# Optimization experiments

Hardware: AMD Instinct MI355X
Metric: run time of the kernel (lower is better)

## Reference

```python
import jax, jax.numpy as jnp
import numpy as np

DIM = 128
HEADS = 4
DIM_HEAD = 32
N_EMBD = HEADS * DIM_HEAD  # 128
SCALE = DIM_HEAD ** -0.5


def conv2d(x, w, b):
    # NCHW conv, 3x3, stride 1, SAME padding (= padding=1 in torch)
    out = jax.lax.conv_general_dilated(
        x, w, window_strides=(1, 1), padding='SAME',
        dimension_numbers=('NCHW', 'OIHW', 'NCHW'))
    return out + b[None, :, None, None]


def conv_block(x, w1, b1, w2, b2):
    # Conv -> ReLU -> Conv (the to_q/to_k/to_v pattern)
    return conv2d(jax.nn.relu(conv2d(x, w1, b1)), w2, b2)


def setup_inputs() -> dict:
    key = jax.random.key(0)
    ks = jax.random.split(key, 20)
    B, C, S = 4, DIM, 32
    H, W = 128, 512
    wscale = 0.05

    def cw(k, cout, cin):
        return jax.random.normal(k, (cout, cin, 3, 3), jnp.float32) * wscale

    inp = {
        'x': jax.random.normal(ks[0], (B, C, S, S), jnp.float32),
        'y': jax.random.normal(ks[1], (B, C, H, W), jnp.float32),
        'u': jax.random.randint(ks[2], (B, S, S), 0, W),
        'q_w1': cw(ks[3], N_EMBD, DIM), 'q_b1': jnp.zeros((N_EMBD,), jnp.float32),
        'q_w2': cw(ks[4], N_EMBD, N_EMBD), 'q_b2': jnp.zeros((N_EMBD,), jnp.float32),
        'k_w1': cw(ks[5], N_EMBD, DIM), 'k_b1': jnp.zeros((N_EMBD,), jnp.float32),
        'k_w2': cw(ks[6], N_EMBD, N_EMBD), 'k_b2': jnp.zeros((N_EMBD,), jnp.float32),
        'v_w1': cw(ks[7], N_EMBD, DIM), 'v_b1': jnp.zeros((N_EMBD,), jnp.float32),
        'v_w2': cw(ks[8], N_EMBD, N_EMBD), 'v_b2': jnp.zeros((N_EMBD,), jnp.float32),
        'proj_w': cw(ks[9], DIM, N_EMBD), 'proj_b': jnp.zeros((DIM,), jnp.float32),
    }
    return inp


def reference(x, y, u, q_w1, q_b1, q_w2, q_b2, k_w1, k_b1, k_w2, k_b2,
              v_w1, v_b1, v_w2, v_b2, proj_w, proj_b):
    B, C, S, _ = x.shape
    _, _, H, W = y.shape
    SS = S * S

    # Q from the (B,C,S,S) query grid -> (B, S^2, n_embd)
    q = conv_block(x, q_w1, q_b1, q_w2, q_b2).reshape(B, N_EMBD, SS).transpose(0, 2, 1)

    # K, V from the (B,C,H,W) map
    k = conv_block(y, k_w1, k_b1, k_w2, k_b2)  # (B, E, H, W)
    v = conv_block(y, v_w1, v_b1, v_w2, v_b2)

    # Gather columns of K/V along W per query index u (clamped)
    uc = jnp.clip(u, 0, W - 1).astype(jnp.int32).reshape(B, 1, 1, SS)
    ks = jnp.take_along_axis(k, uc, axis=3).transpose(0, 3, 2, 1)  # (B, SS, H, E)
    vs = jnp.take_along_axis(v, uc, axis=3).transpose(0, 3, 2, 1)  # (B, SS, H, E)

    # Per-query attention over the H axis
    dot = SCALE * jnp.einsum('bqe,bqhe->bqh', q, ks)  # (B, SS, H)
    attn = jax.nn.softmax(dot, axis=-1)
    a = jnp.einsum('bqh,bqhe->bqe', attn, vs)  # (B, SS, E)

    a = a.transpose(0, 2, 1).reshape(B, N_EMBD, S, S)
    z = jax.nn.relu(conv2d(a, proj_w, proj_b))  # (B, DIM, S, S)
    return z
```

## Files before the change

kernel.cpp:

```cpp
#include <hip/hip_runtime.h>
#include <stdint.h>

typedef __attribute__((ext_vector_type(16))) float f32x16;
typedef __attribute__((ext_vector_type(8))) short s16x8;

__device__ inline short bf16b(float f) {
  uint32_t x = __float_as_uint(f);
  return (short)((x + 0x7fffu + ((x >> 16) & 1u)) >> 16);
}
__device__ inline float bfu(uint16_t u) { return __uint_as_float(((uint32_t)u) << 16); }

__device__ inline void gll16(const void* g, void* l) {
  __builtin_amdgcn_global_load_lds((const __attribute__((address_space(1))) void*)g,
                                   (__attribute__((address_space(3))) void*)l, 16, 0, 0);
}

__global__ __launch_bounds__(256) void packw_k(
    const float* w0, const float* w1, const float* w2, const float* w3,
    const float* w4, const float* w5, const float* w6, s16x8* dst) {
  const float* srcs[7] = {w0, w1, w2, w3, w4, w5, w6};
  const int widx = blockIdx.y;
  const float* src = srcs[widx];
  const int gid = blockIdx.x * 256 + threadIdx.x;
  const int lane = gid & 63, frag = gid >> 6;
  const int nblk = frag & 3, ks = (frag >> 2) & 1, chunk = (frag >> 3) & 3, tap = frag >> 5;
  const int co = nblk * 32 + (lane & 31);
  const int cib = chunk * 32 + ks * 16 + (lane >> 5) * 8;
  s16x8 v;
#pragma unroll
  for (int j = 0; j < 8; ++j)
    v[j] = bf16b(src[((size_t)co * 128 + cib + j) * 9 + tap]);
  dst[(size_t)widx * 18432 + (size_t)frag * 64 + lane] = v;
}

template <int TW>
__global__ __launch_bounds__(256) void nchw2nhwc_k(
    const float* __restrict__ in, uint16_t* __restrict__ out, int H, int W) {
  __shared__ float tile[128][TW + 1];
  const int b = blockIdx.z, h = blockIdx.y, w0 = blockIdx.x * TW;
  for (int idx = threadIdx.x; idx < 128 * TW; idx += 256) {
    int c = idx / TW, w = idx - c * TW;
    tile[c][w] = in[(((size_t)b * 128 + c) * H + h) * W + w0 + w];
  }
  __syncthreads();
  for (int idx = threadIdx.x; idx < TW * 16; idx += 256) {
    int w = idx >> 4, cg = idx & 15;
    s16x8 v;
#pragma unroll
    for (int j = 0; j < 8; ++j) v[j] = bf16b(tile[cg * 8 + j][w]);
    *reinterpret_cast<s16x8*>(out + ((((size_t)b * H + h) * W + w0 + w) << 7) + cg * 8) = v;
  }
}

template <int OMODE, bool RELU, typename Tout>
__global__ __launch_bounds__(256, 2) void convmf2_k(
    const uint16_t* __restrict__ in, const s16x8* __restrict__ wpk,
    const float* __restrict__ bias, Tout* __restrict__ out,
    const uint16_t* __restrict__ zp, int H, int W) {
  constexpr int CP = 34, RPCP = 10 * 34;
  constexpr int SLOTS = 4 * RPCP;
  constexpr int SPT = 6;
  __shared__ s16x8 lds[2][SPT * 256];
  const int b = blockIdx.z, r0 = blockIdx.y * 8, c0 = blockIdx.x * 32;
  const int tid = threadIdx.x, lane = tid & 63;
  const int wv = tid >> 6, wm = wv >> 1, wn = wv & 1;
  const int wbase = tid & 192;

  const uint16_t* gsrc[SPT];
#pragma unroll
  for (int i = 0; i < SPT; ++i) {
    const int s = tid + i * 256;
    const int kq = s / RPCP;
    const int rem = s - kq * RPCP;
    const int r = rem / CP, c = rem - r * CP;
    const int gr = r0 + r - 1, gc = c0 + c - 1;
    const bool ok = (s < SLOTS) && gr >= 0 && gr < H && gc >= 0 && gc < W;
    gsrc[i] = ok ? (in + (((size_t)b * H + gr) * W + gc) * 128 + kq * 8) : zp;
  }

#pragma unroll
  for (int i = 0; i < SPT; ++i) gll16(gsrc[i], &lds[0][wbase + i * 256]);

  f32x16 acc[4][2];
#pragma unroll
  for (int i = 0; i < 4; ++i)
#pragma unroll
    for (int j = 0; j < 2; ++j)
#pragma unroll
      for (int r = 0; r < 16; ++r) acc[i][j][r] = 0.f;

  const int rowb = wm * 4 * CP + (lane >> 5) * RPCP + (lane & 31);
  __syncthreads();

#pragma unroll 1
  for (int chunk = 0; chunk < 4; ++chunk) {
    const int cb = chunk & 1;
    if (chunk < 3) {
#pragma unroll
      for (int i = 0; i < SPT; ++i)
        gll16(gsrc[i] + (chunk + 1) * 32, &lds[cb ^ 1][wbase + i * 256]);
    }
    const s16x8* __restrict__ Lb = &lds[cb][rowb];
    const s16x8* __restrict__ wpc = wpk + ((size_t)chunk * 8 + wn * 2) * 64 + lane;
    s16x8 bwA[2], bwB[2];
    bwA[0] = wpc[0]; bwA[1] = wpc[64];
#pragma unroll
    for (int t9 = 0; t9 < 18; ++t9) {
      const int tap = t9 >> 1, ks = t9 & 1;
      const int ky = tap / 3, kx = tap - ky * 3;
      if (t9 < 17) {
        const int tn = t9 + 1, tapn = tn >> 1, ksn = tn & 1;
        s16x8* nx = (t9 & 1) ? bwA : bwB;
        nx[0] = wpc[tapn * 2048 + ksn * 256];
        nx[1] = wpc[tapn * 2048 + ksn * 256 + 64];
      }
      const s16x8* cw = (t9 & 1) ? bwB : bwA;
#pragma unroll
      for (int mf = 0; mf < 4; ++mf) {
        const s16x8 av = Lb[ks * (2 * RPCP) + (mf + ky) * CP + kx];
        acc[mf][0] = __builtin_amdgcn_mfma_f32_32x32x16_bf16(av, cw[0], acc[mf][0], 0, 0, 0);
        acc[mf][1] = __builtin_amdgcn_mfma_f32_32x32x16_bf16(av, cw[1], acc[mf][1], 0, 0, 0);
      }
    }
    if (chunk < 3) __syncthreads();
  }

#pragma unroll
  for (int nf = 0; nf < 2; ++nf) {
    const int co = wn * 64 + nf * 32 + (lane & 31);
    const float bv = bias[co];
#pragma unroll
    for (int mf = 0; mf < 4; ++mf) {
      const int gr = r0 + wm * 4 + mf;
#pragma unroll
      for (int reg = 0; reg < 16; ++reg) {
        const int gc = c0 + (reg & 3) + 8 * (reg >> 2) + 4 * (lane >> 5);
        float v = acc[mf][nf][reg] + bv;
        if (RELU) v = fmaxf(v, 0.f);
        size_t idx;
        if (OMODE == 0)      idx = (((size_t)b * H + gr) * W + gc) * 128 + co;
        else if (OMODE == 1) idx = (((size_t)b * W + gc) * H + gr) * 128 + co;
        else                 idx = (((size_t)b * 128 + co) * H + gr) * W + gc;
        if constexpr (sizeof(Tout) == 2) ((uint16_t*)out)[idx] = (uint16_t)bf16b(v);
        else out[idx] = v;
      }
    }
  }
}

__global__ __launch_bounds__(128) void attn_dot_k(
    const float* __restrict__ qg, const uint16_t* __restrict__ Kg,
    const int* __restrict__ u, float* __restrict__ pout) {
  const int bs = blockIdx.x;
  const int b = bs >> 10;
  const int tid = threadIdx.x;
  __shared__ float sq[128], sd[128];
  sq[tid] = qg[(size_t)bs * 128 + tid];
  int w = u[bs]; w = w < 0 ? 0 : (w > 511 ? 511 : w);
  __syncthreads();
  const uint32_t* kp = reinterpret_cast<const uint32_t*>(
      Kg + (((size_t)b * 512 + w) * 128 + tid) * 128);
  float acc = 0.f;
#pragma unroll 8
  for (int i = 0; i < 64; ++i) {
    uint32_t v = kp[i];
    acc = fmaf(sq[2 * i],     __uint_as_float(v << 16), acc);
    acc = fmaf(sq[2 * i + 1], __uint_as_float(v & 0xffff0000u), acc);
  }
  sd[tid] = acc * 0.17677669529663687f;
  __syncthreads();
  float mx = -1e30f;
  for (int i = 0; i < 128; ++i) mx = fmaxf(mx, sd[i]);
  float e = expf(sd[tid] - mx);
  __syncthreads();
  sd[tid] = e;
  __syncthreads();
  float sum = 0.f;
  for (int i = 0; i < 128; ++i) sum += sd[i];
  pout[(size_t)bs * 128 + tid] = e / sum;
}

__global__ __launch_bounds__(128) void attn_pv_k(
    const float* __restrict__ pin, const uint16_t* __restrict__ Vg,
    const int* __restrict__ u, uint16_t* __restrict__ aout) {
  const int bs = blockIdx.x;
  const int b = bs >> 10;
  const int tid = threadIdx.x;
  __shared__ float sp[128];
  sp[tid] = pin[(size_t)bs * 128 + tid];
  int w = u[bs]; w = w < 0 ? 0 : (w > 511 ? 511 : w);
  __syncthreads();
  const uint16_t* vp = Vg + ((size_t)b * 512 + w) * 16384 + tid;
  float acc = 0.f;
#pragma unroll 8
  for (int h = 0; h < 128; ++h)
    acc = fmaf(sp[h], bfu(vp[h * 128]), acc);
  aout[(size_t)bs * 128 + tid] = (uint16_t)bf16b(acc);
}

extern "C" void kernel_launch(void* const* d_in, const int* in_sizes, int n_in,
                              void* d_out, int out_size, void* d_ws, size_t ws_size,
                              hipStream_t stream) {
  const float* x      = (const float*)d_in[0];
  const float* y      = (const float*)d_in[1];
  const int*   u      = (const int*)d_in[2];
  const float* q_w1   = (const float*)d_in[3];
  const float* q_b1   = (const float*)d_in[4];
  const float* q_w2   = (const float*)d_in[5];
  const float* q_b2   = (const float*)d_in[6];
  const float* k_w1   = (const float*)d_in[7];
  const float* k_b1   = (const float*)d_in[8];
  const float* k_w2   = (const float*)d_in[9];
  const float* k_b2   = (const float*)d_in[10];
  const float* v_w1   = (const float*)d_in[11];
  const float* v_b1   = (const float*)d_in[12];
  const float* v_w2   = (const float*)d_in[13];
  const float* v_b2   = (const float*)d_in[14];
  const float* proj_w = (const float*)d_in[15];
  const float* proj_b = (const float*)d_in[16];
  float* out = (float*)d_out;

  char* ws = (char*)d_ws;
  const size_t MB = 1 << 20;
  const size_t BIG = 64 * MB;
  const bool tierB = ws_size >= 203 * MB;
  uint16_t* A  = (uint16_t*)ws;
  uint16_t* Bb = (uint16_t*)(ws + BIG);
  uint16_t* KV = tierB ? (uint16_t*)(ws + 2 * BIG) : A;
  char* sm = ws + (tierB ? 3 : 2) * BIG;
  float*    qg  = (float*)sm;
  float*    pb  = (float*)(sm + 2 * MB);
  uint16_t* xbf = (uint16_t*)(sm + 4 * MB);
  uint16_t* t1  = (uint16_t*)(sm + 5 * MB);
  uint16_t* ab  = (uint16_t*)(sm + 6 * MB);
  s16x8*    wpk = (s16x8*)(sm + 7 * MB);
  uint16_t* zp  = (uint16_t*)(sm + 10 * MB);

  hipMemsetAsync(zp, 0, 1024, stream);
  packw_k<<<dim3(72, 7), 256, 0, stream>>>(q_w1, q_w2, k_w1, k_w2, v_w1, v_w2, proj_w, wpk);
  nchw2nhwc_k<32><<<dim3(1, 32, 4), 256, 0, stream>>>(x, xbf, 32, 32);
  nchw2nhwc_k<64><<<dim3(8, 128, 4), 256, 0, stream>>>(y, A, 128, 512);
  convmf2_k<0, true,  uint16_t><<<dim3(1, 4, 4), 256, 0, stream>>>(xbf, wpk + 0 * 18432, q_b1, t1, zp, 32, 32);
  convmf2_k<0, false, float   ><<<dim3(1, 4, 4), 256, 0, stream>>>(t1,  wpk + 1 * 18432, q_b2, qg, zp, 32, 32);
  convmf2_k<0, true,  uint16_t><<<dim3(16, 16, 4), 256, 0, stream>>>(A,  wpk + 2 * 18432, k_b1, Bb, zp, 128, 512);
  convmf2_k<1, false, uint16_t><<<dim3(16, 16, 4), 256, 0, stream>>>(Bb, wpk + 3 * 18432, k_b2, KV, zp, 128, 512);
  attn_dot_k<<<dim3(4096), 128, 0, stream>>>(qg, KV, u, pb);
  if (!tierB) nchw2nhwc_k<64><<<dim3(8, 128, 4), 256, 0, stream>>>(y, A, 128, 512);
  convmf2_k<0, true,  uint16_t><<<dim3(16, 16, 4), 256, 0, stream>>>(A,  wpk + 4 * 18432, v_b1, Bb, zp, 128, 512);
  convmf2_k<1, false, uint16_t><<<dim3(16, 16, 4), 256, 0, stream>>>(Bb, wpk + 5 * 18432, v_b2, KV, zp, 128, 512);
  attn_pv_k<<<dim3(4096), 128, 0, stream>>>(pb, KV, u, ab);
  convmf2_k<3, true, float><<<dim3(1, 4, 4), 256, 0, stream>>>(ab, wpk + 6 * 18432, proj_b, out, zp, 32, 32);
}
```

Before: 488.3 us.

## Restructure conv tile: per-wave 32 out-channels, register-cached weights and A rows

```diff
diff --git a/kernel.cpp b/kernel.cpp
--- a/kernel.cpp
+++ b/kernel.cpp
@@ -53,17 +53,16 @@
 }
 
 template <int OMODE, bool RELU, typename Tout>
-__global__ __launch_bounds__(256, 2) void convmf2_k(
+__global__ __launch_bounds__(256, 2) void convmf3_k(
     const uint16_t* __restrict__ in, const s16x8* __restrict__ wpk,
     const float* __restrict__ bias, Tout* __restrict__ out,
     const uint16_t* __restrict__ zp, int H, int W) {
-  constexpr int CP = 34, RPCP = 10 * 34;
+  constexpr int CP = 34, RP = 6, RPCP = RP * CP;
   constexpr int SLOTS = 4 * RPCP;
-  constexpr int SPT = 6;
+  constexpr int SPT = 4;
   __shared__ s16x8 lds[2][SPT * 256];
-  const int b = blockIdx.z, r0 = blockIdx.y * 8, c0 = blockIdx.x * 32;
-  const int tid = threadIdx.x, lane = tid & 63;
-  const int wv = tid >> 6, wm = wv >> 1, wn = wv & 1;
+  const int b = blockIdx.z, r0 = blockIdx.y * 4, c0 = blockIdx.x * 32;
+  const int tid = threadIdx.x, lane = tid & 63, wn = tid >> 6;
   const int wbase = tid & 192;
 
   const uint16_t* gsrc[SPT];
@@ -78,21 +77,27 @@
     gsrc[i] = ok ? (in + (((size_t)b * H + gr) * W + gc) * 128 + kq * 8) : zp;
   }
 
+  const s16x8* __restrict__ wbl = wpk + wn * 64 + lane;
+  s16x8 wf[18];
+#pragma unroll
+  for (int t9 = 0; t9 < 18; ++t9) {
+    const int tap = t9 >> 1, ks = t9 & 1;
+    wf[t9] = wbl[(tap * 8 + ks) * 256];
+  }
+
 #pragma unroll
   for (int i = 0; i < SPT; ++i) gll16(gsrc[i], &lds[0][wbase + i * 256]);
 
-  f32x16 acc[4][2];
+  f32x16 acc[4];
 #pragma unroll
   for (int i = 0; i < 4; ++i)
 #pragma unroll
-    for (int j = 0; j < 2; ++j)
-#pragma unroll
-      for (int r = 0; r < 16; ++r) acc[i][j][r] = 0.f;
-
-  const int rowb = wm * 4 * CP + (lane >> 5) * RPCP + (lane & 31);
-  __syncthreads();
-
-#pragma unroll 1
+    for (int r = 0; r < 16; ++r) acc[i][r] = 0.f;
+
+  const int abase = (lane >> 5) * RPCP + (lane & 31);
+  __syncthreads();
+
+#pragma unroll
   for (int chunk = 0; chunk < 4; ++chunk) {
     const int cb = chunk & 1;
     if (chunk < 3) {
@@ -100,50 +105,59 @@
       for (int i = 0; i < SPT; ++i)
         gll16(gsrc[i] + (chunk + 1) * 32, &lds[cb ^ 1][wbase + i * 256]);
     }
-    const s16x8* __restrict__ Lb = &lds[cb][rowb];
-    const s16x8* __restrict__ wpc = wpk + ((size_t)chunk * 8 + wn * 2) * 64 + lane;
-    s16x8 bwA[2], bwB[2];
-    bwA[0] = wpc[0]; bwA[1] = wpc[64];
-#pragma unroll
-    for (int t9 = 0; t9 < 18; ++t9) {
-      const int tap = t9 >> 1, ks = t9 & 1;
-      const int ky = tap / 3, kx = tap - ky * 3;
-      if (t9 < 17) {
-        const int tn = t9 + 1, tapn = tn >> 1, ksn = tn & 1;
-        s16x8* nx = (t9 & 1) ? bwA : bwB;
-        nx[0] = wpc[tapn * 2048 + ksn * 256];
-        nx[1] = wpc[tapn * 2048 + ksn * 256 + 64];
+    const s16x8* __restrict__ Lb = &lds[cb][abase];
+    s16x8 arA[6], arB[6];
+#pragma unroll
+    for (int r = 0; r < 6; ++r) arA[r] = Lb[r * CP];
+#pragma unroll
+    for (int j = 0; j < 6; ++j) {
+      const int ks = j / 3, kx = j - ks * 3;
+      if (j < 5) {
+        const int jn = j + 1, ksn = jn / 3, kxn = jn - ksn * 3;
+#pragma unroll
+        for (int r = 0; r < 6; ++r) {
+          s16x8 v = Lb[ksn * 2 * RPCP + r * CP + kxn];
+          if (j & 1) arA[r] = v; else arB[r] = v;
+        }
       }
-      const s16x8* cw = (t9 & 1) ? bwB : bwA;
-#pragma unroll
-      for (int mf = 0; mf < 4; ++mf) {
-        const s16x8 av = Lb[ks * (2 * RPCP) + (mf + ky) * CP + kx];
-        acc[mf][0] = __builtin_amdgcn_mfma_f32_32x32x16_bf16(av, cw[0], acc[mf][0], 0, 0, 0);
-        acc[mf][1] = __builtin_amdgcn_mfma_f32_32x32x16_bf16(av, cw[1], acc[mf][1], 0, 0, 0);
+      __builtin_amdgcn_s_setprio(1);
+#pragma unroll
+      for (int ky = 0; ky < 3; ++ky) {
+        const int t9 = (ky * 3 + kx) * 2 + ks;
+#pragma unroll
+        for (int mf = 0; mf < 4; ++mf) {
+          const s16x8 a = (j & 1) ? arB[mf + ky] : arA[mf + ky];
+          acc[mf] = __builtin_amdgcn_mfma_f32_32x32x16_bf16(a, wf[t9], acc[mf], 0, 0, 0);
+        }
+      }
+      __builtin_amdgcn_s_setprio(0);
+      if (chunk < 3) {
+#pragma unroll
+        for (int ky = 0; ky < 3; ++ky) {
+          const int tap = ky * 3 + kx;
+          wf[tap * 2 + ks] = wbl[((tap * 4 + chunk + 1) * 2 + ks) * 256];
+        }
       }
     }
     if (chunk < 3) __syncthreads();
   }
 
-#pragma unroll
-  for (int nf = 0; nf < 2; ++nf) {
-    const int co = wn * 64 + nf * 32 + (lane & 31);
-    const float bv = bias[co];
-#pragma unroll
-    for (int mf = 0; mf < 4; ++mf) {
-      const int gr = r0 + wm * 4 + mf;
-#pragma unroll
-      for (int reg = 0; reg < 16; ++reg) {
-        const int gc = c0 + (reg & 3) + 8 * (reg >> 2) + 4 * (lane >> 5);
-        float v = acc[mf][nf][reg] + bv;
-        if (RELU) v = fmaxf(v, 0.f);
-        size_t idx;
-        if (OMODE == 0)      idx = (((size_t)b * H + gr) * W + gc) * 128 + co;
-        else if (OMODE == 1) idx = (((size_t)b * W + gc) * H + gr) * 128 + co;
-        else                 idx = (((size_t)b * 128 + co) * H + gr) * W + gc;
-        if constexpr (sizeof(Tout) == 2) ((uint16_t*)out)[idx] = (uint16_t)bf16b(v);
-        else out[idx] = v;
-      }
+  const int co = wn * 32 + (lane & 31);
+  const float bv = bias[co];
+#pragma unroll
+  for (int mf = 0; mf < 4; ++mf) {
+    const int gr = r0 + mf;
+#pragma unroll
+    for (int reg = 0; reg < 16; ++reg) {
+      const int gc = c0 + (reg & 3) + 8 * (reg >> 2) + 4 * (lane >> 5);
+      float v = acc[mf][reg] + bv;
+      if (RELU) v = fmaxf(v, 0.f);
+      size_t idx;
+      if (OMODE == 0)      idx = (((size_t)b * H + gr) * W + gc) * 128 + co;
+      else if (OMODE == 1) idx = (((size_t)b * W + gc) * H + gr) * 128 + co;
+      else                 idx = (((size_t)b * 128 + co) * H + gr) * W + gc;
+      if constexpr (sizeof(Tout) == 2) ((uint16_t*)out)[idx] = (uint16_t)bf16b(v);
+      else out[idx] = v;
     }
   }
 }
@@ -240,14 +254,14 @@
   packw_k<<<dim3(72, 7), 256, 0, stream>>>(q_w1, q_w2, k_w1, k_w2, v_w1, v_w2, proj_w, wpk);
   nchw2nhwc_k<32><<<dim3(1, 32, 4), 256, 0, stream>>>(x, xbf, 32, 32);
   nchw2nhwc_k<64><<<dim3(8, 128, 4), 256, 0, stream>>>(y, A, 128, 512);
-  convmf2_k<0, true,  uint16_t><<<dim3(1, 4, 4), 256, 0, stream>>>(xbf, wpk + 0 * 18432, q_b1, t1, zp, 32, 32);
-  convmf2_k<0, false, float   ><<<dim3(1, 4, 4), 256, 0, stream>>>(t1,  wpk + 1 * 18432, q_b2, qg, zp, 32, 32);
-  convmf2_k<0, true,  uint16_t><<<dim3(16, 16, 4), 256, 0, stream>>>(A,  wpk + 2 * 18432, k_b1, Bb, zp, 128, 512);
-  convmf2_k<1, false, uint16_t><<<dim3(16, 16, 4), 256, 0, stream>>>(Bb, wpk + 3 * 18432, k_b2, KV, zp, 128, 512);
+  convmf3_k<0, true,  uint16_t><<<dim3(1, 8, 4), 256, 0, stream>>>(xbf, wpk + 0 * 18432, q_b1, t1, zp, 32, 32);
+  convmf3_k<0, false, float   ><<<dim3(1, 8, 4), 256, 0, stream>>>(t1,  wpk + 1 * 18432, q_b2, qg, zp, 32, 32);
+  convmf3_k<0, true,  uint16_t><<<dim3(16, 32, 4), 256, 0, stream>>>(A,  wpk + 2 * 18432, k_b1, Bb, zp, 128, 512);
+  convmf3_k<1, false, uint16_t><<<dim3(16, 32, 4), 256, 0, stream>>>(Bb, wpk + 3 * 18432, k_b2, KV, zp, 128, 512);
   attn_dot_k<<<dim3(4096), 128, 0, stream>>>(qg, KV, u, pb);
   if (!tierB) nchw2nhwc_k<64><<<dim3(8, 128, 4), 256, 0, stream>>>(y, A, 128, 512);
-  convmf2_k<0, true,  uint16_t><<<dim3(16, 16, 4), 256, 0, stream>>>(A,  wpk + 4 * 18432, v_b1, Bb, zp, 128, 512);
-  convmf2_k<1, false, uint16_t><<<dim3(16, 16, 4), 256, 0, stream>>>(Bb, wpk + 5 * 18432, v_b2, KV, zp, 128, 512);
+  convmf3_k<0, true,  uint16_t><<<dim3(16, 32, 4), 256, 0, stream>>>(A,  wpk + 4 * 18432, v_b1, Bb, zp, 128, 512);
+  convmf3_k<1, false, uint16_t><<<dim3(16, 32, 4), 256, 0, stream>>>(Bb, wpk + 5 * 18432, v_b2, KV, zp, 128, 512);
   attn_pv_k<<<dim3(4096), 128, 0, stream>>>(pb, KV, u, ab);
-  convmf2_k<3, true, float><<<dim3(1, 4, 4), 256, 0, stream>>>(ab, wpk + 6 * 18432, proj_b, out, zp, 32, 32);
-}
+  convmf3_k<3, true, float><<<dim3(1, 8, 4), 256, 0, stream>>>(ab, wpk + 6 * 18432, proj_b, out, zp, 32, 32);
+}
```

Measured after the change: 430.0 us. -11.9%, faster.
